# Performance work log

Hardware: AMD Instinct MI355X
Metric: run time of the kernel (lower is better)

The kernel has to match this reference:

```python
import jax, jax.numpy as jnp
import numpy as np

N_QUBITS = 4
N_LAYERS = 2
DIM = 2 ** N_QUBITS


def _cnot_perm(c, t, n=N_QUBITS):
    # statevector index bit for wire w is at shift (n-1-w)
    idx = np.arange(2 ** n)
    cbit = (idx >> (n - 1 - c)) & 1
    return np.where(cbit == 1, idx ^ (1 << (n - 1 - t)), idx)


def _apply_cnot(state, c, t):
    # state: [B, 2,2,2,2]; CNOT is a basis permutation (its own inverse)
    B = state.shape[0]
    flat = state.reshape(B, DIM)
    return flat[:, _cnot_perm(c, t)].reshape(state.shape)


def _apply_1q(state, U, wire):
    # shared 2x2 gate U on given wire
    st = jnp.moveaxis(state, wire + 1, -1)
    st = jnp.einsum('b...a,ca->b...c', st, U)
    return jnp.moveaxis(st, -1, wire + 1)


def _quantum_circuit(z, weights):
    """AngleEmbedding(RY) + StronglyEntanglingLayers, PauliZ expvals.
    z: [B, n_qubits] angles, weights: [L, n_qubits, 3]. Returns [B, n_qubits]."""
    n = N_QUBITS
    B = z.shape[0]
    state = jnp.zeros((B, DIM), jnp.complex64).at[:, 0].set(1.0)
    state = state.reshape((B,) + (2,) * n)
    # Angle embedding: batched RY(z_w) on each wire
    for w in range(n):
        a = z[:, w] * 0.5
        c, s = jnp.cos(a), jnp.sin(a)
        U = jnp.stack([jnp.stack([c, -s], -1), jnp.stack([s, c], -1)], -2)  # [B,2,2]
        st = jnp.moveaxis(state, w + 1, -1)
        st = jnp.einsum('b...a,bca->b...c', st, U.astype(jnp.complex64))
        state = jnp.moveaxis(st, -1, w + 1)
    # StronglyEntanglingLayers
    for l in range(N_LAYERS):
        for w in range(n):
            phi, theta, omega = weights[l, w, 0], weights[l, w, 1], weights[l, w, 2]
            ct, st_ = jnp.cos(theta * 0.5), jnp.sin(theta * 0.5)
            e_m = jnp.exp(-0.5j * (phi + omega).astype(jnp.complex64))
            e_d = jnp.exp(0.5j * (phi - omega).astype(jnp.complex64))
            U = jnp.stack([
                jnp.stack([e_m * ct, -e_d * st_]),
                jnp.stack([jnp.conj(e_d) * st_, jnp.conj(e_m) * ct]),
            ])  # Rot(phi,theta,omega) = RZ(omega) RY(theta) RZ(phi)
            state = _apply_1q(state, U, w)
        r = (l % (n - 1)) + 1
        for w in range(n):
            state = _apply_cnot(state, w, (w + r) % n)
    probs = state.real ** 2 + state.imag ** 2  # [B,2,2,2,2]
    evs = []
    rest = tuple(range(1, n))
    for w in range(n):
        p = jnp.moveaxis(probs, w + 1, 1)
        evs.append(jnp.sum(p[:, 0], axis=rest) - jnp.sum(p[:, 1], axis=rest))
    return jnp.stack(evs, -1)


def setup_inputs() -> dict:
    key = jax.random.key(0)
    ks = jax.random.split(key, 6)
    B, C, H, W = 16, 256, 128, 128
    return {
        'x': jax.random.normal(ks[0], (B, C, H, W), jnp.float32),
        'enc_w': jax.random.normal(ks[1], (N_QUBITS, C), jnp.float32) / np.sqrt(C),
        'enc_b': jax.random.normal(ks[2], (N_QUBITS,), jnp.float32) * 0.01,
        'qweights': jax.random.uniform(ks[3], (N_LAYERS, N_QUBITS, 3), jnp.float32, 0.0, 2.0 * np.pi),
        'proj_w': jax.random.normal(ks[4], (C, N_QUBITS), jnp.float32) / np.sqrt(N_QUBITS),
        'proj_b': jax.random.normal(ks[5], (C,), jnp.float32) * 0.01,
    }


def reference(x, enc_w, enc_b, qweights, proj_w, proj_b):
    pooled = jnp.mean(x, axis=(2, 3))                      # AdaptiveAvgPool2d(1)+Flatten -> [B,C]
    z = jnp.tanh(pooled @ enc_w.T + enc_b)                 # [B, n_qubits]
    refined = _quantum_circuit(z, qweights)                # [B, n_qubits]
    gates = jax.nn.sigmoid(refined @ proj_w.T + proj_b)    # [B, C]
    return x + x * gates[:, :, None, None]
```

## Files before the change

### kernel.cpp

```cpp
#include <hip/hip_runtime.h>
#include <math.h>

#define NQ 4
#define NL 2
#define DIM 16
#define BATCH 16
#define CH 256
#define HW 16384
#define SPB 4
#define NBLK (BATCH * CH / SPB)

typedef float floatx4 __attribute__((ext_vector_type(4)));

__global__ void pool_kernel(const float* __restrict__ x, float* __restrict__ pooled) {
    const int bc = blockIdx.x;
    const floatx4* x4 = (const floatx4*)(x + (size_t)bc * HW);
    const int tid = threadIdx.x;
    float s = 0.f;
#pragma unroll
    for (int k = 0; k < 16; ++k) {
        floatx4 v = __builtin_nontemporal_load(&x4[tid + k * 256]);
        s += v.x + v.y + v.z + v.w;
    }
#pragma unroll
    for (int off = 32; off > 0; off >>= 1) s += __shfl_down(s, off, 64);
    __shared__ float partial[4];
    if ((tid & 63) == 0) partial[tid >> 6] = s;
    __syncthreads();
    if (tid == 0)
        pooled[bc] = (partial[0] + partial[1] + partial[2] + partial[3]) * (1.0f / HW);
}

__global__ void fused_gate_scale(
    const float* __restrict__ x,
    const float* __restrict__ enc_w,
    const float* __restrict__ enc_b,
    const float* __restrict__ qw,
    const float* __restrict__ proj_w,
    const float* __restrict__ proj_b,
    const float* __restrict__ pooled,
    float* __restrict__ out)
{
    const int tid = threadIdx.x;
    const int slice0 = blockIdx.x * SPB;
    const int b = slice0 >> 8;

    __shared__ float sz[NQ];
    __shared__ float sevs[NQ];
    __shared__ float sgate[SPB];

    {
        const int wid = tid >> 6, lane = tid & 63;
        const float* prow = pooled + b * CH;
        float acc = 0.f;
#pragma unroll
        for (int j = 0; j < 4; ++j) {
            const int c = lane * 4 + j;
            acc += prow[c] * enc_w[wid * CH + c];
        }
#pragma unroll
        for (int off = 32; off > 0; off >>= 1) acc += __shfl_down(acc, off, 64);
        if (lane == 0) sz[wid] = tanhf(acc + enc_b[wid]);
    }
    __syncthreads();

    if (tid == 0) {
        float re[DIM], im[DIM];
#pragma unroll
        for (int i = 0; i < DIM; ++i) { re[i] = 0.f; im[i] = 0.f; }
        re[0] = 1.f;

        for (int w = 0; w < NQ; ++w) {
            const float a = sz[w] * 0.5f;
            const float cc = cosf(a), ss = sinf(a);
            const int m = 1 << (3 - w);
#pragma unroll
            for (int i = 0; i < DIM; ++i) {
                if (i & m) continue;
                const int j = i | m;
                const float r0 = cc * re[i] - ss * re[j];
                const float i0 = cc * im[i] - ss * im[j];
                const float r1 = ss * re[i] + cc * re[j];
                const float i1 = ss * im[i] + cc * im[j];
                re[i] = r0; im[i] = i0; re[j] = r1; im[j] = i1;
            }
        }

        for (int l = 0; l < NL; ++l) {
            for (int w = 0; w < NQ; ++w) {
                const float phi = qw[(l * NQ + w) * 3 + 0];
                const float th  = qw[(l * NQ + w) * 3 + 1];
                const float om  = qw[(l * NQ + w) * 3 + 2];
                const float ct = cosf(0.5f * th), st = sinf(0.5f * th);
                const float am = -0.5f * (phi + om);
                const float ad =  0.5f * (phi - om);
                const float emr = cosf(am), emi = sinf(am);
                const float edr = cosf(ad), edi = sinf(ad);
                const float u00r =  emr * ct, u00i =  emi * ct;
                const float u01r = -edr * st, u01i = -edi * st;
                const float u10r =  edr * st, u10i = -edi * st;
                const float u11r =  emr * ct, u11i = -emi * ct;
                const int m = 1 << (3 - w);
#pragma unroll
                for (int i = 0; i < DIM; ++i) {
                    if (i & m) continue;
                    const int j = i | m;
                    const float ar = re[i], ai = im[i], br = re[j], bi = im[j];
                    re[i] = u00r * ar - u00i * ai + u01r * br - u01i * bi;
                    im[i] = u00r * ai + u00i * ar + u01r * bi + u01i * br;
                    re[j] = u10r * ar - u10i * ai + u11r * br - u11i * bi;
                    im[j] = u10r * ai + u10i * ar + u11r * bi + u11i * br;
                }
            }
            const int r = (l % (NQ - 1)) + 1;
            for (int w = 0; w < NQ; ++w) {
                const int t = (w + r) % NQ;
                const int cm = 1 << (3 - w);
                const int tm = 1 << (3 - t);
#pragma unroll
                for (int i = 0; i < DIM; ++i) {
                    if ((i & cm) && !(i & tm)) {
                        const int j = i | tm;
                        float tr = re[i]; re[i] = re[j]; re[j] = tr;
                        float ti = im[i]; im[i] = im[j]; im[j] = ti;
                    }
                }
            }
        }

        float p[DIM];
#pragma unroll
        for (int i = 0; i < DIM; ++i) p[i] = re[i] * re[i] + im[i] * im[i];
        for (int w = 0; w < NQ; ++w) {
            const int m = 1 << (3 - w);
            float ev = 0.f;
#pragma unroll
            for (int i = 0; i < DIM; ++i) ev += (i & m) ? -p[i] : p[i];
            sevs[w] = ev;
        }
    }
    __syncthreads();

    if (tid < SPB) {
        const int c = (slice0 & 255) + tid;
        const float acc = sevs[0] * proj_w[c * NQ + 0] + sevs[1] * proj_w[c * NQ + 1] +
                          sevs[2] * proj_w[c * NQ + 2] + sevs[3] * proj_w[c * NQ + 3] +
                          proj_b[c];
        sgate[tid] = 1.f + 1.f / (1.f + expf(-acc));
    }
    __syncthreads();

    for (int s = 0; s < SPB; ++s) {
        const float gt = sgate[s];
        const floatx4* x4 = (const floatx4*)(x + (size_t)(slice0 + s) * HW);
        floatx4* o4 = (floatx4*)(out + (size_t)(slice0 + s) * HW);
        floatx4 v[16];
#pragma unroll
        for (int k = 0; k < 16; ++k) v[k] = __builtin_nontemporal_load(&x4[tid + k * 256]);
#pragma unroll
        for (int k = 0; k < 16; ++k) {
            v[k] *= gt;
            __builtin_nontemporal_store(v[k], &o4[tid + k * 256]);
        }
    }
}

extern "C" void kernel_launch(void* const* d_in, const int* in_sizes, int n_in,
                              void* d_out, int out_size, void* d_ws, size_t ws_size,
                              hipStream_t stream) {
    const float* x      = (const float*)d_in[0];
    const float* enc_w  = (const float*)d_in[1];
    const float* enc_b  = (const float*)d_in[2];
    const float* qw     = (const float*)d_in[3];
    const float* proj_w = (const float*)d_in[4];
    const float* proj_b = (const float*)d_in[5];
    float* out = (float*)d_out;
    float* pooled = (float*)d_ws;

    pool_kernel<<<BATCH * CH, 256, 0, stream>>>(x, pooled);
    fused_gate_scale<<<NBLK, 256, 0, stream>>>(x, enc_w, enc_b, qw,
                                               proj_w, proj_b, pooled, out);
}
```

Before: 173.8 us.

## Fuse pooling and gating into one persistent kernel with grid barrier

Merges the pooling kernel and the gate/scale kernel into a single launch of 512 blocks, each handling 8 channel slices. A global atomic counter acts as a grid-wide barrier between the pooling phase and the gating phase. Each block keeps its first two slices in registers across the barrier so they need not be read from memory twice, and the pooling loads no longer carry the nontemporal hint, so other slices may still be in L2/MALL when re-read. The risks are deadlock if the 512 blocks cannot all be resident at once, high register pressure from holding 32 float4 values per thread, and an extra memset launch.

```diff
diff --git a/kernel.cpp b/kernel.cpp
--- a/kernel.cpp
+++ b/kernel.cpp
@@ -7,60 +7,98 @@
 #define BATCH 16
 #define CH 256
 #define HW 16384
-#define SPB 4
-#define NBLK (BATCH * CH / SPB)
+#define NBLK 512
+#define SPB 8
 
 typedef float floatx4 __attribute__((ext_vector_type(4)));
 
-__global__ void pool_kernel(const float* __restrict__ x, float* __restrict__ pooled) {
-    const int bc = blockIdx.x;
-    const floatx4* x4 = (const floatx4*)(x + (size_t)bc * HW);
-    const int tid = threadIdx.x;
-    float s = 0.f;
-#pragma unroll
-    for (int k = 0; k < 16; ++k) {
-        floatx4 v = __builtin_nontemporal_load(&x4[tid + k * 256]);
-        s += v.x + v.y + v.z + v.w;
-    }
-#pragma unroll
-    for (int off = 32; off > 0; off >>= 1) s += __shfl_down(s, off, 64);
-    __shared__ float partial[4];
-    if ((tid & 63) == 0) partial[tid >> 6] = s;
-    __syncthreads();
-    if (tid == 0)
-        pooled[bc] = (partial[0] + partial[1] + partial[2] + partial[3]) * (1.0f / HW);
-}
-
-__global__ void fused_gate_scale(
+__global__ __launch_bounds__(256, 2) void fused_all(
     const float* __restrict__ x,
     const float* __restrict__ enc_w,
     const float* __restrict__ enc_b,
     const float* __restrict__ qw,
     const float* __restrict__ proj_w,
     const float* __restrict__ proj_b,
-    const float* __restrict__ pooled,
-    float* __restrict__ out)
+    float* __restrict__ out,
+    float* __restrict__ pooled,
+    unsigned* __restrict__ ctr)
 {
     const int tid = threadIdx.x;
     const int slice0 = blockIdx.x * SPB;
     const int b = slice0 >> 8;
 
+    __shared__ float partial[4];
     __shared__ float sz[NQ];
     __shared__ float sevs[NQ];
     __shared__ float sgate[SPB];
 
+    floatx4 v0[16], v1[16];
     {
-        const int wid = tid >> 6, lane = tid & 63;
+        const floatx4* x0 = (const floatx4*)(x + (size_t)(slice0 + 0) * HW);
+        const floatx4* x1 = (const floatx4*)(x + (size_t)(slice0 + 1) * HW);
+#pragma unroll
+        for (int k = 0; k < 16; ++k) v0[k] = x0[tid + k * 256];
+#pragma unroll
+        for (int k = 0; k < 16; ++k) v1[k] = x1[tid + k * 256];
+        float s0 = 0.f, s1 = 0.f;
+#pragma unroll
+        for (int k = 0; k < 16; ++k) { s0 += v0[k].x + v0[k].y + v0[k].z + v0[k].w; }
+#pragma unroll
+        for (int k = 0; k < 16; ++k) { s1 += v1[k].x + v1[k].y + v1[k].z + v1[k].w; }
+#pragma unroll
+        for (int off = 32; off > 0; off >>= 1) s0 += __shfl_down(s0, off, 64);
+        if ((tid & 63) == 0) partial[tid >> 6] = s0;
+        __syncthreads();
+        if (tid == 0)
+            pooled[slice0 + 0] = (partial[0] + partial[1] + partial[2] + partial[3]) * (1.f / HW);
+        __syncthreads();
+#pragma unroll
+        for (int off = 32; off > 0; off >>= 1) s1 += __shfl_down(s1, off, 64);
+        if ((tid & 63) == 0) partial[tid >> 6] = s1;
+        __syncthreads();
+        if (tid == 0)
+            pooled[slice0 + 1] = (partial[0] + partial[1] + partial[2] + partial[3]) * (1.f / HW);
+        __syncthreads();
+    }
+    for (int s = 2; s < SPB; ++s) {
+        const floatx4* xp = (const floatx4*)(x + (size_t)(slice0 + s) * HW);
+        float acc = 0.f;
+#pragma unroll
+        for (int k = 0; k < 16; ++k) {
+            floatx4 t = xp[tid + k * 256];
+            acc += t.x + t.y + t.z + t.w;
+        }
+#pragma unroll
+        for (int off = 32; off > 0; off >>= 1) acc += __shfl_down(acc, off, 64);
+        if ((tid & 63) == 0) partial[tid >> 6] = acc;
+        __syncthreads();
+        if (tid == 0)
+            pooled[slice0 + s] = (partial[0] + partial[1] + partial[2] + partial[3]) * (1.f / HW);
+        __syncthreads();
+    }
+
+    __syncthreads();
+    if (tid == 0) {
+        __threadfence();
+        __hip_atomic_fetch_add(ctr, 1u, __ATOMIC_ACQ_REL, __HIP_MEMORY_SCOPE_AGENT);
+        while (__hip_atomic_load(ctr, __ATOMIC_ACQUIRE, __HIP_MEMORY_SCOPE_AGENT) < (unsigned)NBLK)
+            __builtin_amdgcn_s_sleep(8);
+        __threadfence();
+    }
+    __syncthreads();
+
+    {
+        const int q = tid >> 6, lane = tid & 63;
         const float* prow = pooled + b * CH;
         float acc = 0.f;
 #pragma unroll
         for (int j = 0; j < 4; ++j) {
             const int c = lane * 4 + j;
-            acc += prow[c] * enc_w[wid * CH + c];
+            acc += prow[c] * enc_w[q * CH + c];
         }
 #pragma unroll
         for (int off = 32; off > 0; off >>= 1) acc += __shfl_down(acc, off, 64);
-        if (lane == 0) sz[wid] = tanhf(acc + enc_b[wid]);
+        if (lane == 0) sz[q] = tanhf(acc + enc_b[q]);
     }
     __syncthreads();
 
@@ -85,7 +123,6 @@
                 re[i] = r0; im[i] = i0; re[j] = r1; im[j] = i1;
             }
         }
-
         for (int l = 0; l < NL; ++l) {
             for (int w = 0; w < NQ; ++w) {
                 const float phi = qw[(l * NQ + w) * 3 + 0];
@@ -127,7 +164,6 @@
                 }
             }
         }
-
         float p[DIM];
 #pragma unroll
         for (int i = 0; i < DIM; ++i) p[i] = re[i] * re[i] + im[i] * im[i];
@@ -150,17 +186,32 @@
     }
     __syncthreads();
 
-    for (int s = 0; s < SPB; ++s) {
-        const float gt = sgate[s];
-        const floatx4* x4 = (const floatx4*)(x + (size_t)(slice0 + s) * HW);
-        floatx4* o4 = (floatx4*)(out + (size_t)(slice0 + s) * HW);
-        floatx4 v[16];
-#pragma unroll
-        for (int k = 0; k < 16; ++k) v[k] = __builtin_nontemporal_load(&x4[tid + k * 256]);
-#pragma unroll
-        for (int k = 0; k < 16; ++k) {
-            v[k] *= gt;
-            __builtin_nontemporal_store(v[k], &o4[tid + k * 256]);
+    {
+        floatx4* o0 = (floatx4*)(out + (size_t)(slice0 + 0) * HW);
+        floatx4* o1 = (floatx4*)(out + (size_t)(slice0 + 1) * HW);
+        const float g0 = sgate[0], g1 = sgate[1];
+#pragma unroll
+        for (int k = 0; k < 16; ++k) {
+            floatx4 t = v0[k] * g0;
+            __builtin_nontemporal_store(t, &o0[tid + k * 256]);
+        }
+#pragma unroll
+        for (int k = 0; k < 16; ++k) {
+            floatx4 t = v1[k] * g1;
+            __builtin_nontemporal_store(t, &o1[tid + k * 256]);
+        }
+    }
+    for (int s = 2; s < SPB; ++s) {
+        const float g = sgate[s];
+        const floatx4* xp = (const floatx4*)(x + (size_t)(slice0 + s) * HW);
+        floatx4* op = (floatx4*)(out + (size_t)(slice0 + s) * HW);
+        floatx4 t[16];
+#pragma unroll
+        for (int k = 0; k < 16; ++k) t[k] = xp[tid + k * 256];
+#pragma unroll
+        for (int k = 0; k < 16; ++k) {
+            floatx4 w = t[k] * g;
+            __builtin_nontemporal_store(w, &op[tid + k * 256]);
         }
     }
 }
@@ -175,9 +226,11 @@
     const float* proj_w = (const float*)d_in[4];
     const float* proj_b = (const float*)d_in[5];
     float* out = (float*)d_out;
+
     float* pooled = (float*)d_ws;
-
-    pool_kernel<<<BATCH * CH, 256, 0, stream>>>(x, pooled);
-    fused_gate_scale<<<NBLK, 256, 0, stream>>>(x, enc_w, enc_b, qw,
-                                               proj_w, proj_b, pooled, out);
+    unsigned* ctr = (unsigned*)(pooled + BATCH * CH);
+
+    hipMemsetAsync(ctr, 0, sizeof(unsigned), stream);
+    fused_all<<<NBLK, 256, 0, stream>>>(x, enc_w, enc_b, qw, proj_w, proj_b,
+                                        out, pooled, ctr);
 }
```

New measurement: 211.9 us. 1.22x slower.

## Fuse pooling and gating into one persistent kernel with a grid barrier

Applied to the files above, without the earlier changes.

Merges the pooling and gate-scale kernels into a single launch. Each block pools its four channel slices, publishes the means, then waits on a global atomic counter until all blocks are done before computing the gate. Part of x is kept in registers and LDS so it does not have to be re-read from HBM for the scale pass. This relies on all 1024 blocks being co-resident, enforced through launch bounds and LDS usage, and deadlocks if they are not. It also adds a memset launch and the cost of spinning at the barrier.

```diff
diff --git a/kernel.cpp b/kernel.cpp
--- a/kernel.cpp
+++ b/kernel.cpp
@@ -7,60 +7,89 @@
 #define BATCH 16
 #define CH 256
 #define HW 16384
+#define NBLK 1024
 #define SPB 4
-#define NBLK (BATCH * CH / SPB)
 
 typedef float floatx4 __attribute__((ext_vector_type(4)));
 
-__global__ void pool_kernel(const float* __restrict__ x, float* __restrict__ pooled) {
-    const int bc = blockIdx.x;
-    const floatx4* x4 = (const floatx4*)(x + (size_t)bc * HW);
-    const int tid = threadIdx.x;
-    float s = 0.f;
-#pragma unroll
-    for (int k = 0; k < 16; ++k) {
-        floatx4 v = __builtin_nontemporal_load(&x4[tid + k * 256]);
-        s += v.x + v.y + v.z + v.w;
-    }
-#pragma unroll
-    for (int off = 32; off > 0; off >>= 1) s += __shfl_down(s, off, 64);
-    __shared__ float partial[4];
-    if ((tid & 63) == 0) partial[tid >> 6] = s;
-    __syncthreads();
-    if (tid == 0)
-        pooled[bc] = (partial[0] + partial[1] + partial[2] + partial[3]) * (1.0f / HW);
-}
-
-__global__ void fused_gate_scale(
+__global__ __launch_bounds__(256, 4) void fused_all(
     const float* __restrict__ x,
     const float* __restrict__ enc_w,
     const float* __restrict__ enc_b,
     const float* __restrict__ qw,
     const float* __restrict__ proj_w,
     const float* __restrict__ proj_b,
-    const float* __restrict__ pooled,
-    float* __restrict__ out)
+    float* __restrict__ out,
+    float* __restrict__ pooled,
+    unsigned* __restrict__ ctr)
 {
     const int tid = threadIdx.x;
     const int slice0 = blockIdx.x * SPB;
     const int b = slice0 >> 8;
 
+    __shared__ floatx4 lds1[8 * 256];
+    __shared__ float part[SPB][4];
     __shared__ float sz[NQ];
     __shared__ float sevs[NQ];
     __shared__ float sgate[SPB];
 
+    const floatx4* xs0 = (const floatx4*)(x + (size_t)(slice0 + 0) * HW);
+    const floatx4* xs1 = (const floatx4*)(x + (size_t)(slice0 + 1) * HW);
+    const floatx4* xs2 = (const floatx4*)(x + (size_t)(slice0 + 2) * HW);
+    const floatx4* xs3 = (const floatx4*)(x + (size_t)(slice0 + 3) * HW);
+
+    floatx4 v0[16];
+    float a0 = 0.f, a1 = 0.f, a2 = 0.f, a3 = 0.f;
+#pragma unroll
+    for (int k = 0; k < 16; ++k) {
+        v0[k] = xs0[tid + k * 256];
+        floatx4 t1 = xs1[tid + k * 256];
+        floatx4 t2 = xs2[tid + k * 256];
+        floatx4 t3 = xs3[tid + k * 256];
+        if (k < 8) lds1[k * 256 + tid] = t1;
+        a0 += v0[k].x + v0[k].y + v0[k].z + v0[k].w;
+        a1 += t1.x + t1.y + t1.z + t1.w;
+        a2 += t2.x + t2.y + t2.z + t2.w;
+        a3 += t3.x + t3.y + t3.z + t3.w;
+    }
     {
         const int wid = tid >> 6, lane = tid & 63;
+        float av[SPB] = {a0, a1, a2, a3};
+#pragma unroll
+        for (int s = 0; s < SPB; ++s) {
+            float r = av[s];
+#pragma unroll
+            for (int off = 32; off > 0; off >>= 1) r += __shfl_down(r, off, 64);
+            if (lane == 0) part[s][wid] = r;
+        }
+    }
+    __syncthreads();
+    if (tid < SPB)
+        pooled[slice0 + tid] =
+            (part[tid][0] + part[tid][1] + part[tid][2] + part[tid][3]) * (1.f / HW);
+
+    __syncthreads();
+    if (tid == 0) {
+        __threadfence();
+        __hip_atomic_fetch_add(ctr, 1u, __ATOMIC_ACQ_REL, __HIP_MEMORY_SCOPE_AGENT);
+        while (__hip_atomic_load(ctr, __ATOMIC_ACQUIRE, __HIP_MEMORY_SCOPE_AGENT) < (unsigned)NBLK)
+            __builtin_amdgcn_s_sleep(8);
+        __threadfence();
+    }
+    __syncthreads();
+
+    {
+        const int q = tid >> 6, lane = tid & 63;
         const float* prow = pooled + b * CH;
         float acc = 0.f;
 #pragma unroll
         for (int j = 0; j < 4; ++j) {
             const int c = lane * 4 + j;
-            acc += prow[c] * enc_w[wid * CH + c];
+            acc += prow[c] * enc_w[q * CH + c];
         }
 #pragma unroll
         for (int off = 32; off > 0; off >>= 1) acc += __shfl_down(acc, off, 64);
-        if (lane == 0) sz[wid] = tanhf(acc + enc_b[wid]);
+        if (lane == 0) sz[q] = tanhf(acc + enc_b[q]);
     }
     __syncthreads();
 
@@ -85,7 +114,6 @@
                 re[i] = r0; im[i] = i0; re[j] = r1; im[j] = i1;
             }
         }
-
         for (int l = 0; l < NL; ++l) {
             for (int w = 0; w < NQ; ++w) {
                 const float phi = qw[(l * NQ + w) * 3 + 0];
@@ -127,7 +155,6 @@
                 }
             }
         }
-
         float p[DIM];
 #pragma unroll
         for (int i = 0; i < DIM; ++i) p[i] = re[i] * re[i] + im[i] * im[i];
@@ -150,18 +177,32 @@
     }
     __syncthreads();
 
-    for (int s = 0; s < SPB; ++s) {
-        const float gt = sgate[s];
-        const floatx4* x4 = (const floatx4*)(x + (size_t)(slice0 + s) * HW);
-        floatx4* o4 = (floatx4*)(out + (size_t)(slice0 + s) * HW);
-        floatx4 v[16];
-#pragma unroll
-        for (int k = 0; k < 16; ++k) v[k] = __builtin_nontemporal_load(&x4[tid + k * 256]);
-#pragma unroll
-        for (int k = 0; k < 16; ++k) {
-            v[k] *= gt;
-            __builtin_nontemporal_store(v[k], &o4[tid + k * 256]);
-        }
+    const float g0 = sgate[0], g1 = sgate[1], g2 = sgate[2], g3 = sgate[3];
+    floatx4* os0 = (floatx4*)(out + (size_t)(slice0 + 0) * HW);
+    floatx4* os1 = (floatx4*)(out + (size_t)(slice0 + 1) * HW);
+    floatx4* os2 = (floatx4*)(out + (size_t)(slice0 + 2) * HW);
+    floatx4* os3 = (floatx4*)(out + (size_t)(slice0 + 3) * HW);
+
+#pragma unroll
+    for (int k = 0; k < 16; ++k)
+        __builtin_nontemporal_store(v0[k] * g0, &os0[tid + k * 256]);
+#pragma unroll
+    for (int k = 0; k < 8; ++k) {
+        floatx4 t = lds1[k * 256 + tid];
+        __builtin_nontemporal_store(t * g1, &os1[tid + k * 256]);
+    }
+#pragma unroll
+    for (int k = 0; k < 8; ++k) {
+        floatx4 u1 = xs1[tid + (k + 8) * 256];
+        floatx4 u2 = xs2[tid + k * 256];
+        floatx4 u2b = xs2[tid + (k + 8) * 256];
+        floatx4 u3 = xs3[tid + k * 256];
+        floatx4 u3b = xs3[tid + (k + 8) * 256];
+        __builtin_nontemporal_store(u1 * g1, &os1[tid + (k + 8) * 256]);
+        __builtin_nontemporal_store(u2 * g2, &os2[tid + k * 256]);
+        __builtin_nontemporal_store(u2b * g2, &os2[tid + (k + 8) * 256]);
+        __builtin_nontemporal_store(u3 * g3, &os3[tid + k * 256]);
+        __builtin_nontemporal_store(u3b * g3, &os3[tid + (k + 8) * 256]);
     }
 }
 
@@ -175,9 +216,11 @@
     const float* proj_w = (const float*)d_in[4];
     const float* proj_b = (const float*)d_in[5];
     float* out = (float*)d_out;
+
     float* pooled = (float*)d_ws;
-
-    pool_kernel<<<BATCH * CH, 256, 0, stream>>>(x, pooled);
-    fused_gate_scale<<<NBLK, 256, 0, stream>>>(x, enc_w, enc_b, qw,
-                                               proj_w, proj_b, pooled, out);
+    unsigned* ctr = (unsigned*)(pooled + BATCH * CH);
+
+    hipMemsetAsync(ctr, 0, sizeof(unsigned), stream);
+    fused_all<<<NBLK, 256, 0, stream>>>(x, enc_w, enc_b, qw, proj_w, proj_b,
+                                        out, pooled, ctr);
 }
```

Result: slower. 472.5 us (+171.9%).

## Split gate computation into its own kernel and reverse-order scale pass for cache reuse

Applied to the files above, without the earlier changes.

The quantum-circuit gate computation moves into a small per-batch kernel that writes all gate values to workspace, so it is no longer redundantly recomputed in every scale block. The scale kernel visits slices in reverse order and the pool kernel and scale pass now use normal rather than nontemporal loads, so the tail of x read last by the pool pass may still be in cache (MI355X Infinity Cache) when the scale pass starts. This adds a third kernel launch and a serial gate step between the pool and scale passes.

```diff
diff --git a/kernel.cpp b/kernel.cpp
--- a/kernel.cpp
+++ b/kernel.cpp
@@ -7,8 +7,6 @@
 #define BATCH 16
 #define CH 256
 #define HW 16384
-#define SPB 4
-#define NBLK (BATCH * CH / SPB)
 
 typedef float floatx4 __attribute__((ext_vector_type(4)));
 
@@ -19,7 +17,7 @@
     float s = 0.f;
 #pragma unroll
     for (int k = 0; k < 16; ++k) {
-        floatx4 v = __builtin_nontemporal_load(&x4[tid + k * 256]);
+        floatx4 v = x4[tid + k * 256];
         s += v.x + v.y + v.z + v.w;
     }
 #pragma unroll
@@ -31,36 +29,31 @@
         pooled[bc] = (partial[0] + partial[1] + partial[2] + partial[3]) * (1.0f / HW);
 }
 
-__global__ void fused_gate_scale(
-    const float* __restrict__ x,
-    const float* __restrict__ enc_w,
-    const float* __restrict__ enc_b,
-    const float* __restrict__ qw,
-    const float* __restrict__ proj_w,
-    const float* __restrict__ proj_b,
-    const float* __restrict__ pooled,
-    float* __restrict__ out)
-{
+__global__ void gate_kernel16(const float* __restrict__ pooled,
+                              const float* __restrict__ enc_w,
+                              const float* __restrict__ enc_b,
+                              const float* __restrict__ qw,
+                              const float* __restrict__ proj_w,
+                              const float* __restrict__ proj_b,
+                              float* __restrict__ gates1p) {
+    const int b = blockIdx.x;
     const int tid = threadIdx.x;
-    const int slice0 = blockIdx.x * SPB;
-    const int b = slice0 >> 8;
 
     __shared__ float sz[NQ];
     __shared__ float sevs[NQ];
-    __shared__ float sgate[SPB];
 
     {
-        const int wid = tid >> 6, lane = tid & 63;
+        const int q = tid >> 6, lane = tid & 63;
         const float* prow = pooled + b * CH;
         float acc = 0.f;
 #pragma unroll
         for (int j = 0; j < 4; ++j) {
             const int c = lane * 4 + j;
-            acc += prow[c] * enc_w[wid * CH + c];
+            acc += prow[c] * enc_w[q * CH + c];
         }
 #pragma unroll
         for (int off = 32; off > 0; off >>= 1) acc += __shfl_down(acc, off, 64);
-        if (lane == 0) sz[wid] = tanhf(acc + enc_b[wid]);
+        if (lane == 0) sz[q] = tanhf(acc + enc_b[q]);
     }
     __syncthreads();
 
@@ -85,7 +78,6 @@
                 re[i] = r0; im[i] = i0; re[j] = r1; im[j] = i1;
             }
         }
-
         for (int l = 0; l < NL; ++l) {
             for (int w = 0; w < NQ; ++w) {
                 const float phi = qw[(l * NQ + w) * 3 + 0];
@@ -127,7 +119,6 @@
                 }
             }
         }
-
         float p[DIM];
 #pragma unroll
         for (int i = 0; i < DIM; ++i) p[i] = re[i] * re[i] + im[i] * im[i];
@@ -141,27 +132,30 @@
     }
     __syncthreads();
 
-    if (tid < SPB) {
-        const int c = (slice0 & 255) + tid;
+    {
+        const int c = tid;
         const float acc = sevs[0] * proj_w[c * NQ + 0] + sevs[1] * proj_w[c * NQ + 1] +
                           sevs[2] * proj_w[c * NQ + 2] + sevs[3] * proj_w[c * NQ + 3] +
                           proj_b[c];
-        sgate[tid] = 1.f + 1.f / (1.f + expf(-acc));
+        gates1p[b * CH + c] = 1.f + 1.f / (1.f + expf(-acc));
     }
-    __syncthreads();
+}
 
-    for (int s = 0; s < SPB; ++s) {
-        const float gt = sgate[s];
-        const floatx4* x4 = (const floatx4*)(x + (size_t)(slice0 + s) * HW);
-        floatx4* o4 = (floatx4*)(out + (size_t)(slice0 + s) * HW);
-        floatx4 v[16];
+__global__ void scale_kernel(const float* __restrict__ x,
+                             const float* __restrict__ gates1p,
+                             float* __restrict__ out) {
+    const int slice = 4095 - blockIdx.x;
+    const int tid = threadIdx.x;
+    const floatx4* x4 = (const floatx4*)(x + (size_t)slice * HW);
+    floatx4* o4 = (floatx4*)(out + (size_t)slice * HW);
+    const float g = gates1p[slice];
+    floatx4 v[16];
 #pragma unroll
-        for (int k = 0; k < 16; ++k) v[k] = __builtin_nontemporal_load(&x4[tid + k * 256]);
+    for (int k = 0; k < 16; ++k) v[k] = x4[tid + k * 256];
 #pragma unroll
-        for (int k = 0; k < 16; ++k) {
-            v[k] *= gt;
-            __builtin_nontemporal_store(v[k], &o4[tid + k * 256]);
-        }
+    for (int k = 0; k < 16; ++k) {
+        v[k] *= g;
+        __builtin_nontemporal_store(v[k], &o4[tid + k * 256]);
     }
 }
 
@@ -175,9 +169,12 @@
     const float* proj_w = (const float*)d_in[4];
     const float* proj_b = (const float*)d_in[5];
     float* out = (float*)d_out;
-    float* pooled = (float*)d_ws;
+
+    float* pooled  = (float*)d_ws;
+    float* gates1p = pooled + BATCH * CH;
 
     pool_kernel<<<BATCH * CH, 256, 0, stream>>>(x, pooled);
-    fused_gate_scale<<<NBLK, 256, 0, stream>>>(x, enc_w, enc_b, qw,
-                                               proj_w, proj_b, pooled, out);
+    gate_kernel16<<<BATCH, 256, 0, stream>>>(pooled, enc_w, enc_b, qw,
+                                             proj_w, proj_b, gates1p);
+    scale_kernel<<<BATCH * CH, 256, 0, stream>>>(x, gates1p, out);
 }
```

Measured after the change: 144.9 us (median of 2 runs). 1.2x faster.
